# Optimization experiments

Measured on AMD Instinct MI355X. Metric: run time of the kernel, lower is better.

Reference implementation:

```python
import jax, jax.numpy as jnp
import numpy as np

HEADS = 16
DIM_HEAD = 64
DIM = 1024
INNER = HEADS * DIM_HEAD  # 1024
DIM_OUT = 1024


def setup_inputs() -> dict:
    key = jax.random.key(0)
    k1, k2, k3, k4 = jax.random.split(key, 4)
    B, N = 4, 2048
    x = jax.random.normal(k1, (B, N, DIM), dtype=jnp.float32)
    # hk.Linear(inner_dim*3, with_bias=False): weight shape [in, out]
    w_qkv = jax.random.normal(k2, (DIM, INNER * 3), dtype=jnp.float32) / np.sqrt(DIM)
    # hk.Linear(dim_out): weight [INNER, DIM_OUT] + bias
    w_out = jax.random.normal(k3, (INNER, DIM_OUT), dtype=jnp.float32) / np.sqrt(INNER)
    b_out = jax.random.normal(k4, (DIM_OUT,), dtype=jnp.float32) * 0.01
    return {"x": x, "w_qkv": w_qkv, "w_out": w_out, "b_out": b_out}


def reference(x, w_qkv, w_out, b_out):
    B, N, _ = x.shape
    scale = DIM_HEAD ** -0.5
    qkv = x @ w_qkv  # [B, N, 3*INNER]
    q, k, v = jnp.split(qkv, 3, axis=-1)
    # b n (h d) -> b h n d
    split_heads = lambda t: t.reshape(B, N, HEADS, DIM_HEAD).transpose(0, 2, 1, 3)
    q, k, v = split_heads(q), split_heads(k), split_heads(v)
    dots = jnp.einsum('bhid,bhjd->bhij', q, k) * scale  # [B, H, N, N]
    attn = jax.nn.softmax(dots, axis=-1)
    out = jnp.einsum('bhij,bhjd->bhid', attn, v)  # [B, H, N, D]
    out = out.transpose(0, 2, 1, 3).reshape(B, N, INNER)  # b h n d -> b n (h d)
    return out @ w_out + b_out
```

## Files before the change

### kernel.cpp

```cpp
#include <hip/hip_runtime.h>
#include <cstdint>


typedef unsigned short ushort_t;
typedef _Float16 half_t;
typedef half_t half8 __attribute__((ext_vector_type(8)));
typedef half_t half4 __attribute__((ext_vector_type(4)));
typedef __fp16 fp16x2 __attribute__((ext_vector_type(2)));
typedef float floatx4 __attribute__((ext_vector_type(4)));
typedef ushort_t ushort8 __attribute__((ext_vector_type(8)));

#define QSCALE 0.18033688011112043f

__device__ __forceinline__ float bf2f(ushort_t h) {
  union { unsigned int u; float f; } v; v.u = ((unsigned int)h) << 16; return v.f;
}
__device__ __forceinline__ void async_copy16(const void* g, void* l) {
  __builtin_amdgcn_global_load_lds(
      reinterpret_cast<const __attribute__((address_space(1))) unsigned int*>(
          reinterpret_cast<uintptr_t>(g)),
      reinterpret_cast<__attribute__((address_space(3))) unsigned int*>(
          reinterpret_cast<uintptr_t>(l)),
      16, 0, 0);
}
__device__ __forceinline__ void lds_fence() {
  asm volatile("s_waitcnt lgkmcnt(0)" ::: "memory");
}
__device__ __forceinline__ void vm_fence() {
  asm volatile("s_waitcnt vmcnt(0)" ::: "memory");
}

__global__ __launch_bounds__(256) void prep_kernel(
    const void* __restrict__ x_raw, half_t* __restrict__ xb,
    const void* __restrict__ w_qkv_raw, half_t* __restrict__ WTqkv,
    const void* __restrict__ w_out_raw, half_t* __restrict__ WTout,
    const void* __restrict__ b_out_raw, float* __restrict__ bb) {
  __shared__ half_t tile[64][65];
  __shared__ int cnt;
  const int tid = threadIdx.x;
  if (tid == 0) cnt = 0;
  __syncthreads();
  {
    const ushort_t* xs = (const ushort_t*)x_raw;
    int local = 0;
    for (int i = tid; i < 8192; i += 256)
      if ((xs[i] & 0x7F80u) == 0x7F80u) ++local;
    if (local) atomicAdd(&cnt, local);
  }
  __syncthreads();
  const int isf32 = (cnt >= 2) ? 1 : 0;
  const int bid = blockIdx.x;

  if (bid < 4096) {
    const int i0 = (bid * 256 + tid) * 8;
    half8 o;
    if (isf32) {
      const floatx4* s = (const floatx4*)x_raw;
      const floatx4 a = s[(i0 >> 2)];
      const floatx4 b = s[(i0 >> 2) + 1];
#pragma unroll
      for (int j = 0; j < 4; ++j) { o[j] = (half_t)a[j]; o[4 + j] = (half_t)b[j]; }
    } else {
      const ushort8 u = *(const ushort8*)((const ushort_t*)x_raw + i0);
#pragma unroll
      for (int j = 0; j < 8; ++j) o[j] = (half_t)bf2f(u[j]);
    }
    *(half8*)&xb[i0] = o;
  } else if (bid < 5120) {
    const int t = bid - 4096;
    const int bx = t & 63;
    const int by = t >> 6;
    const void* src; half_t* dst; int C, c0;
    if (bx < 48) { src = w_qkv_raw; dst = WTqkv; C = 3072; c0 = bx * 64; }
    else         { src = w_out_raw; dst = WTout; C = 1024; c0 = (bx - 48) * 64; }
    const int R = 1024;
    const int r0 = by * 64;
    const int tx = tid & 63, ty = tid >> 6;
    if (isf32) {
      const float* s = (const float*)src;
      for (int i = ty; i < 64; i += 4) tile[i][tx] = (half_t)s[(size_t)(r0 + i) * C + (c0 + tx)];
    } else {
      const ushort_t* s = (const ushort_t*)src;
      for (int i = ty; i < 64; i += 4) tile[i][tx] = (half_t)bf2f(s[(size_t)(r0 + i) * C + (c0 + tx)]);
    }
    __syncthreads();
    for (int i = ty; i < 64; i += 4) dst[(size_t)(c0 + i) * R + (r0 + tx)] = tile[tx][i];
  } else {
#pragma unroll
    for (int j = 0; j < 4; ++j) {
      const int i = j * 256 + tid;
      bb[i] = isf32 ? ((const float*)b_out_raw)[i] : bf2f(((const ushort_t*)b_out_raw)[i]);
    }
  }
}

__global__ __launch_bounds__(256) void gemm_qkv_kernel(
    const half_t* __restrict__ X, const half_t* __restrict__ WT,
    half_t* __restrict__ Qb, half_t* __restrict__ Kb, half_t* __restrict__ VTb) {
  __shared__ half_t smem[128 * 136];
  half_t* As = smem;
  half_t* Bs = smem + 128 * 64;
  const int tid = threadIdx.x;
  const int wv = tid >> 6, lane = tid & 63;
  const int l15 = lane & 15, quad = lane >> 4;
  const int l7 = l15 & 7;
  const int wm = wv & 1, wn = wv >> 1;
  const int bid = blockIdx.x;
  const int xcd = bid & 7, idx = bid >> 3;
  const int mb = xcd * 8 + (idx & 7);
  const int nb = idx >> 3;
  const int rlo = lane >> 3, ci = lane & 7;
  const int sw_klo = (ci ^ rlo) * 8;

  floatx4 acc[4][4];
  const floatx4 z = {0.f, 0.f, 0.f, 0.f};
#pragma unroll
  for (int mi = 0; mi < 4; ++mi)
#pragma unroll
    for (int ni = 0; ni < 4; ++ni) acc[mi][ni] = z;

  const half_t* Abase = X + (size_t)mb * 128 * 1024;
  const half_t* Bbase = WT + (size_t)nb * 128 * 1024;

  for (int k0 = 0; k0 < 1024; k0 += 64) {
#pragma unroll
    for (int j = 0; j < 4; ++j) {
      const int rb = (wv * 4 + j) * 8;
      async_copy16(Abase + (size_t)(rb + rlo) * 1024 + k0 + sw_klo, &As[rb * 64]);
    }
#pragma unroll
    for (int j = 0; j < 4; ++j) {
      const int rb = (wv * 4 + j) * 8;
      async_copy16(Bbase + (size_t)(rb + rlo) * 1024 + k0 + sw_klo, &Bs[rb * 64]);
    }
    __syncthreads();
#pragma unroll
    for (int ks = 0; ks < 2; ++ks) {
      half8 af[4], bfv[4];
#pragma unroll
      for (int mi = 0; mi < 4; ++mi) {
        const int rr = wm * 64 + mi * 16 + l15;
        af[mi] = *(const half8*)&As[rr * 64 + (((ks * 4 + quad) ^ l7) * 8)];
      }
#pragma unroll
      for (int ni = 0; ni < 4; ++ni) {
        const int rr = wn * 64 + ni * 16 + l15;
        bfv[ni] = *(const half8*)&Bs[rr * 64 + (((ks * 4 + quad) ^ l7) * 8)];
      }
#pragma unroll
      for (int mi = 0; mi < 4; ++mi)
#pragma unroll
        for (int ni = 0; ni < 4; ++ni)
          acc[mi][ni] = __builtin_amdgcn_mfma_f32_16x16x32_f16(af[mi], bfv[ni], acc[mi][ni], 0, 0, 0);
    }
    __syncthreads();
  }

  const int which = nb >> 3;
  if (which != 2) {
    const float sc = (which == 0) ? QSCALE : 1.0f;
#pragma unroll
    for (int mi = 0; mi < 4; ++mi)
#pragma unroll
      for (int ni = 0; ni < 4; ++ni) {
        const int col = wn * 64 + ni * 16 + l15;
#pragma unroll
        for (int r = 0; r < 4; ++r) {
          const int row = wm * 64 + mi * 16 + quad * 4 + r;
          smem[row * 132 + col] = (half_t)(acc[mi][ni][r] * sc);
        }
      }
    __syncthreads();
    half_t* dstB = (which == 0) ? Qb : Kb;
    const int hbase = (nb & 7) * 2;
    const int c2 = lane * 2;
    const int hh = hbase + (c2 >> 6);
    const int dd = c2 & 63;
#pragma unroll 4
    for (int i = 0; i < 32; ++i) {
      const int row = wv * 32 + i;
      const uint32_t val = *(const uint32_t*)&smem[row * 132 + c2];
      const int rowg = mb * 128 + row;
      const int bb = rowg >> 11, nn = rowg & 2047;
      *(uint32_t*)&dstB[(((size_t)(bb * 16 + hh)) * 2048 + nn) * 64 + dd] = val;
    }
  } else {
    const int nb2 = nb - 16;
#pragma unroll
    for (int mi = 0; mi < 4; ++mi)
#pragma unroll
      for (int ni = 0; ni < 4; ++ni) {
        const int nl = wn * 64 + ni * 16 + l15;
#pragma unroll
        for (int r = 0; r < 4; ++r) {
          const int ml = wm * 64 + mi * 16 + quad * 4 + r;
          smem[nl * 136 + ml] = (half_t)acc[mi][ni][r];
        }
      }
    __syncthreads();
    const int bb = mb >> 4;
    const int nn0 = (mb * 128) & 2047;
    const int lane2 = lane * 2;
#pragma unroll 4
    for (int it = 0; it < 32; ++it) {
      const int row = it * 4 + wv;
      const int hh = nb2 * 2 + (row >> 6);
      const int dd = row & 63;
      const int keyoff = lane2 ^ ((dd & 8) ? 4 : 0);
      const uint32_t val = *(const uint32_t*)&smem[row * 136 + lane2];
      *(uint32_t*)&VTb[((size_t)((bb * 16 + hh) * 64 + dd)) * 2048 + nn0 + keyoff] = val;
    }
  }
}

__global__ __launch_bounds__(512) void attn_kernel(
    const half_t* __restrict__ Qb, const half_t* __restrict__ Kb,
    const half_t* __restrict__ VTb, half_t* __restrict__ Ob) {
  __shared__ half_t smem[16384];
  const int tid = threadIdx.x, wv = tid >> 6, lane = tid & 63;
  const int l15 = lane & 15, quad = lane >> 4;
  const int l7 = l15 & 7;
  const int bid = blockIdx.x;
  const int xcd = bid & 7, idx = bid >> 3;
  const int bh = ((idx & 7) << 3) + xcd;
  const int qt = idx >> 3;
  const int bq = bh >> 4, hh = bh & 15;
  const half_t* Qg = Qb + (size_t)bh * 2048 * 64;
  const half_t* Kg = Kb + (size_t)bh * 2048 * 64;
  const half_t* Vg = VTb + (size_t)bh * 64 * 2048;
  const int q0 = qt * 256;
  const int rlo = lane >> 3, ci = lane & 7;
  const int sw_klo = (ci ^ rlo) * 8;

  const int q1 = quad >> 1, qb0 = quad & 1, b3 = (l15 >> 3) & 1;
  int kx[2], vx[4];
#pragma unroll
  for (int ks = 0; ks < 2; ++ks) kx[ks] = ((ks * 4 + quad) ^ l7) * 8;
#pragma unroll
  for (int ki = 0; ki < 4; ++ki)
    vx[ki] = (((ki * 2 + q1) ^ l7) * 8) + ((qb0 ^ b3) * 4);

#pragma unroll
  for (int j = 0; j < 4; ++j) {
    const int rb = (wv * 4 + j) * 8;
    async_copy16(Qg + (size_t)(q0 + rb + rlo) * 64 + sw_klo, &smem[rb * 64]);
  }
  vm_fence();
  half8 aq[2][2];
#pragma unroll
  for (int ks = 0; ks < 2; ++ks)
#pragma unroll
    for (int qi = 0; qi < 2; ++qi) {
      const int rr = wv * 32 + qi * 16 + l15;
      aq[ks][qi] = *(const half8*)&smem[rr * 64 + (((ks * 4 + quad) ^ l7) * 8)];
    }
  __syncthreads();

  floatx4 o_acc[2][4];
  const floatx4 z = {0.f, 0.f, 0.f, 0.f};
  float l_st[2] = {0.f, 0.f};
#pragma unroll
  for (int qi = 0; qi < 2; ++qi)
#pragma unroll
    for (int di = 0; di < 4; ++di) o_acc[qi][di] = z;

  {
    const int rb = wv * 8;
    async_copy16(Kg + (size_t)(rb + rlo) * 64 + sw_klo, &smem[rb * 64]);
    async_copy16(Vg + (size_t)(rb + rlo) * 2048 + sw_klo, &smem[8192 + rb * 64]);
  }

#pragma unroll 2
  for (int t = 0; t < 32; ++t) {
    const int co = (t & 1) * 4096;
    const int po = 4096 - co;
    __syncthreads();
    if (t < 31) {
      const int rb = wv * 8;
      async_copy16(Kg + (size_t)((t + 1) * 64 + rb + rlo) * 64 + sw_klo,
                   &smem[po + rb * 64]);
      async_copy16(Vg + (size_t)(rb + rlo) * 2048 + (t + 1) * 64 + sw_klo,
                   &smem[8192 + po + rb * 64]);
    }
    const half_t* Kc = &smem[co];
    const half_t* Vc = &smem[8192 + co];

    floatx4 s_acc[4][2];
#pragma unroll
    for (int ki = 0; ki < 4; ++ki)
#pragma unroll
      for (int qi = 0; qi < 2; ++qi) s_acc[ki][qi] = z;
#pragma unroll
    for (int ks = 0; ks < 2; ++ks) {
      half8 bk[4];
#pragma unroll
      for (int ki = 0; ki < 4; ++ki)
        bk[ki] = *(const half8*)&Kc[(ki * 16 + l15) * 64 + kx[ks]];
      __builtin_amdgcn_s_setprio(1);
#pragma unroll
      for (int ki = 0; ki < 4; ++ki)
#pragma unroll
        for (int qi = 0; qi < 2; ++qi)
          s_acc[ki][qi] = __builtin_amdgcn_mfma_f32_16x16x32_f16(bk[ki], aq[ks][qi], s_acc[ki][qi], 0, 0, 0);
      __builtin_amdgcn_s_setprio(0);
    }

#pragma unroll
    for (int c = 0; c < 2; ++c) {
      half8 bv[4];
#pragma unroll
      for (int di = 0; di < 4; ++di) {
        union { half4 q[2]; half8 v; } b_;
        b_.q[0] = *(const half4*)&Vc[(di * 16 + l15) * 64 + vx[2 * c]];
        b_.q[1] = *(const half4*)&Vc[(di * 16 + l15) * 64 + vx[2 * c + 1]];
        bv[di] = b_.v;
      }
      union Ap { uint32_t u[4]; half8 h; } apu[2];
#pragma unroll
      for (int kii = 0; kii < 2; ++kii)
#pragma unroll
        for (int qi = 0; qi < 2; ++qi) {
          const int ki = c * 2 + kii;
          const float p0 = __builtin_amdgcn_exp2f(s_acc[ki][qi][0]);
          const float p1 = __builtin_amdgcn_exp2f(s_acc[ki][qi][1]);
          const float p2 = __builtin_amdgcn_exp2f(s_acc[ki][qi][2]);
          const float p3 = __builtin_amdgcn_exp2f(s_acc[ki][qi][3]);
          l_st[qi] += (p0 + p1) + (p2 + p3);
          union { fp16x2 v; uint32_t u; } lo_, hi_;
          lo_.v = __builtin_amdgcn_cvt_pkrtz(p0, p1);
          hi_.v = __builtin_amdgcn_cvt_pkrtz(p2, p3);
          apu[qi].u[kii * 2] = lo_.u;
          apu[qi].u[kii * 2 + 1] = hi_.u;
        }
      __builtin_amdgcn_s_setprio(1);
#pragma unroll
      for (int qi = 0; qi < 2; ++qi)
#pragma unroll
        for (int di = 0; di < 4; ++di)
          o_acc[qi][di] = __builtin_amdgcn_mfma_f32_16x16x32_f16(apu[qi].h, bv[di], o_acc[qi][di], 0, 0, 0);
      __builtin_amdgcn_s_setprio(0);
    }
  }

  float linv[2];
#pragma unroll
  for (int qi = 0; qi < 2; ++qi) {
    float rs = l_st[qi];
    rs += __shfl_xor(rs, 16);
    rs += __shfl_xor(rs, 32);
    linv[qi] = 1.0f / rs;
  }

  __syncthreads();
  const int c2 = (tid & 31) * 2;
  const int rbase = (tid >> 5) & 15;
#pragma unroll
  for (int p = 0; p < 2; ++p) {
    if ((wv >> 2) == p) {
      const int rw = (wv & 3) * 32;
#pragma unroll
      for (int qi = 0; qi < 2; ++qi)
#pragma unroll
        for (int r = 0; r < 4; ++r) {
          const float inv = __shfl(linv[qi], quad * 4 + r);
          const int rowl = rw + qi * 16 + quad * 4 + r;
#pragma unroll
          for (int di = 0; di < 4; ++di)
            smem[rowl * 72 + di * 16 + l15] = (half_t)(o_acc[qi][di][r] * inv);
        }
    }
    __syncthreads();
#pragma unroll 4
    for (int i = 0; i < 8; ++i) {
      const int rowl = i * 16 + rbase;
      const uint32_t val = *(const uint32_t*)&smem[rowl * 72 + c2];
      const int nn = q0 + p * 128 + rowl;
      *(uint32_t*)&Ob[((size_t)(bq * 2048 + nn)) * 1024 + hh * 64 + c2] = val;
    }
    __syncthreads();
  }
}

__global__ __launch_bounds__(256) void gemm_out_kernel(
    const half_t* __restrict__ A, const half_t* __restrict__ WT,
    const float* __restrict__ bias, float* __restrict__ out) {
  __shared__ half_t As[128 * 64];
  __shared__ half_t Bs[128 * 64];
  const int tid = threadIdx.x;
  const int wv = tid >> 6, lane = tid & 63;
  const int l15 = lane & 15, quad = lane >> 4;
  const int l7 = l15 & 7;
  const int wm = wv & 1, wn = wv >> 1;
  const int bid = blockIdx.x;
  const int xcd = bid & 7, idx = bid >> 3;
  const int mb = xcd * 8 + (idx & 7);
  const int nb = idx >> 3;
  const int rlo = lane >> 3, ci = lane & 7;
  const int sw_klo = (ci ^ rlo) * 8;

  floatx4 acc[4][4];
  const floatx4 z = {0.f, 0.f, 0.f, 0.f};
#pragma unroll
  for (int mi = 0; mi < 4; ++mi)
#pragma unroll
    for (int ni = 0; ni < 4; ++ni) acc[mi][ni] = z;

  const half_t* Abase = A + (size_t)mb * 128 * 1024;
  const half_t* Bbase = WT + (size_t)nb * 128 * 1024;

  for (int k0 = 0; k0 < 1024; k0 += 64) {
#pragma unroll
    for (int j = 0; j < 4; ++j) {
      const int rb = (wv * 4 + j) * 8;
      async_copy16(Abase + (size_t)(rb + rlo) * 1024 + k0 + sw_klo, &As[rb * 64]);
    }
#pragma unroll
    for (int j = 0; j < 4; ++j) {
      const int rb = (wv * 4 + j) * 8;
      async_copy16(Bbase + (size_t)(rb + rlo) * 1024 + k0 + sw_klo, &Bs[rb * 64]);
    }
    __syncthreads();
#pragma unroll
    for (int ks = 0; ks < 2; ++ks) {
      half8 af[4], bfv[4];
#pragma unroll
      for (int mi = 0; mi < 4; ++mi) {
        const int rr = wm * 64 + mi * 16 + l15;
        af[mi] = *(const half8*)&As[rr * 64 + (((ks * 4 + quad) ^ l7) * 8)];
      }
#pragma unroll
      for (int ni = 0; ni < 4; ++ni) {
        const int rr = wn * 64 + ni * 16 + l15;
        bfv[ni] = *(const half8*)&Bs[rr * 64 + (((ks * 4 + quad) ^ l7) * 8)];
      }
#pragma unroll
      for (int mi = 0; mi < 4; ++mi)
#pragma unroll
        for (int ni = 0; ni < 4; ++ni)
          acc[mi][ni] = __builtin_amdgcn_mfma_f32_16x16x32_f16(af[mi], bfv[ni], acc[mi][ni], 0, 0, 0);
    }
    __syncthreads();
  }

#pragma unroll
  for (int mi = 0; mi < 4; ++mi) {
#pragma unroll
    for (int ni = 0; ni < 4; ++ni) {
      const int colg = nb * 128 + wn * 64 + ni * 16 + l15;
      const float bs = bias[colg];
#pragma unroll
      for (int r = 0; r < 4; ++r) {
        const int rowg = mb * 128 + wm * 64 + mi * 16 + quad * 4 + r;
        out[(size_t)rowg * 1024 + colg] = acc[mi][ni][r] + bs;
      }
    }
  }
}

extern "C" void kernel_launch(void* const* d_in, const int* in_sizes, int n_in,
                              void* d_out, int out_size, void* d_ws, size_t ws_size,
                              hipStream_t stream) {
  const void* x_raw     = d_in[0];
  const void* w_qkv_raw = d_in[1];
  const void* w_out_raw = d_in[2];
  const void* b_out_raw = d_in[3];
  float* out = (float*)d_out;

  char* ws = (char*)d_ws;
  half_t* xb    = (half_t*)(ws);
  half_t* Qb    = (half_t*)(ws + ((size_t)16 << 20));
  half_t* Kb    = (half_t*)(ws + ((size_t)32 << 20));
  half_t* VTb   = (half_t*)(ws + ((size_t)48 << 20));
  half_t* WTqkv = (half_t*)(ws + ((size_t)64 << 20));
  half_t* WTout = (half_t*)(ws + ((size_t)70 << 20));
  float*  bb    = (float*)(ws + ((size_t)72 << 20));
  half_t* Ob    = xb;

  prep_kernel<<<5121, 256, 0, stream>>>(x_raw, xb, w_qkv_raw, WTqkv,
                                        w_out_raw, WTout, b_out_raw, bb);
  gemm_qkv_kernel<<<1536, 256, 0, stream>>>(xb, WTqkv, Qb, Kb, VTb);
  attn_kernel<<<512, 512, 0, stream>>>(Qb, Kb, VTb, Ob);
  gemm_out_kernel<<<512, 256, 0, stream>>>(Ob, WTout, bb, out);
}
```

Baseline: 267.6 us.

## Rewrite QKV GEMM as 256x256 tile with double-buffered interleaved async loads

The QKV projection GEMM moves from 128x128 tiles with 256 threads to 256x256 tiles with 512 threads. It double-buffers the global-to-LDS async copies, issuing loads for the next K step between the MFMA groups of the current one, and uses setprio around the MFMAs. The epilogue now writes Q/K with 16-byte stores and stages V^T in two halves. The goal is more data reuse per tile and overlap of memory with compute. In exchange it uses 128KB of LDS and many more accumulator registers, and launches only 384 blocks, which may limit occupancy and leave some CUs unevenly loaded.

Result: no change. 265.5 us (-0.8%).

```diff
diff --git a/kernel.cpp b/kernel.cpp
--- a/kernel.cpp
+++ b/kernel.cpp
@@ -94,121 +94,201 @@
   }
 }
 
-__global__ __launch_bounds__(256) void gemm_qkv_kernel(
+__global__ __launch_bounds__(512) void gemm_qkv_kernel(
     const half_t* __restrict__ X, const half_t* __restrict__ WT,
     half_t* __restrict__ Qb, half_t* __restrict__ Kb, half_t* __restrict__ VTb) {
-  __shared__ half_t smem[128 * 136];
-  half_t* As = smem;
-  half_t* Bs = smem + 128 * 64;
+  __shared__ half_t smem[65536];
   const int tid = threadIdx.x;
   const int wv = tid >> 6, lane = tid & 63;
-  const int l15 = lane & 15, quad = lane >> 4;
-  const int l7 = l15 & 7;
+  const int l15 = lane & 15, quad = lane >> 4, l7 = l15 & 7;
   const int wm = wv & 1, wn = wv >> 1;
   const int bid = blockIdx.x;
   const int xcd = bid & 7, idx = bid >> 3;
-  const int mb = xcd * 8 + (idx & 7);
-  const int nb = idx >> 3;
+  const int mb = xcd * 4 + (idx & 3);
+  const int nb = idx >> 2;
   const int rlo = lane >> 3, ci = lane & 7;
   const int sw_klo = (ci ^ rlo) * 8;
-
-  floatx4 acc[4][4];
+  const int rb0 = wv * 16, rb1 = wv * 16 + 8;
+
+  const half_t* Ah[2] = {X + (size_t)(mb * 256) * 1024,
+                         X + (size_t)(mb * 256 + 128) * 1024};
+  const half_t* Bh[2] = {WT + (size_t)(nb * 256) * 1024,
+                         WT + (size_t)(nb * 256 + 128) * 1024};
+
+  floatx4 acc[8][4];
   const floatx4 z = {0.f, 0.f, 0.f, 0.f};
 #pragma unroll
-  for (int mi = 0; mi < 4; ++mi)
+  for (int mi = 0; mi < 8; ++mi)
 #pragma unroll
     for (int ni = 0; ni < 4; ++ni) acc[mi][ni] = z;
 
-  const half_t* Abase = X + (size_t)mb * 128 * 1024;
-  const half_t* Bbase = WT + (size_t)nb * 128 * 1024;
-
-  for (int k0 = 0; k0 < 1024; k0 += 64) {
-#pragma unroll
-    for (int j = 0; j < 4; ++j) {
-      const int rb = (wv * 4 + j) * 8;
-      async_copy16(Abase + (size_t)(rb + rlo) * 1024 + k0 + sw_klo, &As[rb * 64]);
-    }
-#pragma unroll
-    for (int j = 0; j < 4; ++j) {
-      const int rb = (wv * 4 + j) * 8;
-      async_copy16(Bbase + (size_t)(rb + rlo) * 1024 + k0 + sw_klo, &Bs[rb * 64]);
-    }
-    __syncthreads();
-#pragma unroll
-    for (int ks = 0; ks < 2; ++ks) {
-      half8 af[4], bfv[4];
-#pragma unroll
-      for (int mi = 0; mi < 4; ++mi) {
-        const int rr = wm * 64 + mi * 16 + l15;
-        af[mi] = *(const half8*)&As[rr * 64 + (((ks * 4 + quad) ^ l7) * 8)];
-      }
-#pragma unroll
-      for (int ni = 0; ni < 4; ++ni) {
-        const int rr = wn * 64 + ni * 16 + l15;
-        bfv[ni] = *(const half8*)&Bs[rr * 64 + (((ks * 4 + quad) ^ l7) * 8)];
-      }
-#pragma unroll
-      for (int mi = 0; mi < 4; ++mi)
-#pragma unroll
-        for (int ni = 0; ni < 4; ++ni)
-          acc[mi][ni] = __builtin_amdgcn_mfma_f32_16x16x32_f16(af[mi], bfv[ni], acc[mi][ni], 0, 0, 0);
-    }
-    __syncthreads();
-  }
-
-  const int which = nb >> 3;
+#pragma unroll
+  for (int h = 0; h < 2; ++h) {
+    async_copy16(Ah[h] + (size_t)(rb0 + rlo) * 1024 + sw_klo, &smem[h * 8192 + rb0 * 64]);
+    async_copy16(Ah[h] + (size_t)(rb1 + rlo) * 1024 + sw_klo, &smem[h * 8192 + rb1 * 64]);
+  }
+#pragma unroll
+  for (int h = 0; h < 2; ++h) {
+    async_copy16(Bh[h] + (size_t)(rb0 + rlo) * 1024 + sw_klo, &smem[16384 + h * 8192 + rb0 * 64]);
+    async_copy16(Bh[h] + (size_t)(rb1 + rlo) * 1024 + sw_klo, &smem[16384 + h * 8192 + rb1 * 64]);
+  }
+
+#pragma unroll 2
+  for (int u = 0; u < 16; ++u) {
+    const int b = u & 1, bn = b ^ 1;
+    const int kn = ((u + 1) & 15) * 64;
+    const int cb = b * 32768, cn = bn * 32768;
+
+    async_copy16(Ah[0] + (size_t)(rb0 + rlo) * 1024 + kn + sw_klo, &smem[cn + rb0 * 64]);
+    async_copy16(Ah[0] + (size_t)(rb1 + rlo) * 1024 + kn + sw_klo, &smem[cn + rb1 * 64]);
+    asm volatile("s_waitcnt vmcnt(2)" ::: "memory");
+    __builtin_amdgcn_s_barrier();
+    __builtin_amdgcn_sched_barrier(0);
+
+    half8 bf[4][2];
+    const int bbase = cb + 16384 + (wn >> 1) * 8192 + ((wn & 1) * 64) * 64;
+#pragma unroll
+    for (int ni = 0; ni < 4; ++ni)
+#pragma unroll
+      for (int ks = 0; ks < 2; ++ks)
+        bf[ni][ks] = *(const half8*)&smem[bbase + (ni * 16 + l15) * 64 + (((ks * 4 + quad) ^ l7) * 8)];
+    const int abase = cb + wm * 8192;
+    {
+      half8 af[2][2];
+#pragma unroll
+      for (int m2 = 0; m2 < 2; ++m2)
+#pragma unroll
+        for (int ks = 0; ks < 2; ++ks)
+          af[m2][ks] = *(const half8*)&smem[abase + ((0 * 2 + m2) * 16 + l15) * 64 + (((ks * 4 + quad) ^ l7) * 8)];
+      __builtin_amdgcn_s_setprio(1);
+#pragma unroll
+      for (int ks = 0; ks < 2; ++ks)
+#pragma unroll
+        for (int m2 = 0; m2 < 2; ++m2)
+#pragma unroll
+          for (int ni = 0; ni < 4; ++ni)
+            acc[0 * 2 + m2][ni] = __builtin_amdgcn_mfma_f32_16x16x32_f16(af[m2][ks], bf[ni][ks], acc[0 * 2 + m2][ni], 0, 0, 0);
+      __builtin_amdgcn_s_setprio(0);
+    }
+    async_copy16(Ah[1] + (size_t)(rb0 + rlo) * 1024 + kn + sw_klo, &smem[cn + 8192 + rb0 * 64]);
+    async_copy16(Ah[1] + (size_t)(rb1 + rlo) * 1024 + kn + sw_klo, &smem[cn + 8192 + rb1 * 64]);
+    {
+      half8 af[2][2];
+#pragma unroll
+      for (int m2 = 0; m2 < 2; ++m2)
+#pragma unroll
+        for (int ks = 0; ks < 2; ++ks)
+          af[m2][ks] = *(const half8*)&smem[abase + ((1 * 2 + m2) * 16 + l15) * 64 + (((ks * 4 + quad) ^ l7) * 8)];
+      __builtin_amdgcn_s_setprio(1);
+#pragma unroll
+      for (int ks = 0; ks < 2; ++ks)
+#pragma unroll
+        for (int m2 = 0; m2 < 2; ++m2)
+#pragma unroll
+          for (int ni = 0; ni < 4; ++ni)
+            acc[1 * 2 + m2][ni] = __builtin_amdgcn_mfma_f32_16x16x32_f16(af[m2][ks], bf[ni][ks], acc[1 * 2 + m2][ni], 0, 0, 0);
+      __builtin_amdgcn_s_setprio(0);
+    }
+    async_copy16(Bh[0] + (size_t)(rb0 + rlo) * 1024 + kn + sw_klo, &smem[cn + 16384 + rb0 * 64]);
+    async_copy16(Bh[0] + (size_t)(rb1 + rlo) * 1024 + kn + sw_klo, &smem[cn + 16384 + rb1 * 64]);
+    {
+      half8 af[2][2];
+#pragma unroll
+      for (int m2 = 0; m2 < 2; ++m2)
+#pragma unroll
+        for (int ks = 0; ks < 2; ++ks)
+          af[m2][ks] = *(const half8*)&smem[abase + ((2 * 2 + m2) * 16 + l15) * 64 + (((ks * 4 + quad) ^ l7) * 8)];
+      __builtin_amdgcn_s_setprio(1);
+#pragma unroll
+      for (int ks = 0; ks < 2; ++ks)
+#pragma unroll
+        for (int m2 = 0; m2 < 2; ++m2)
+#pragma unroll
+          for (int ni = 0; ni < 4; ++ni)
+            acc[2 * 2 + m2][ni] = __builtin_amdgcn_mfma_f32_16x16x32_f16(af[m2][ks], bf[ni][ks], acc[2 * 2 + m2][ni], 0, 0, 0);
+      __builtin_amdgcn_s_setprio(0);
+    }
+    async_copy16(Bh[1] + (size_t)(rb0 + rlo) * 1024 + kn + sw_klo, &smem[cn + 24576 + rb0 * 64]);
+    async_copy16(Bh[1] + (size_t)(rb1 + rlo) * 1024 + kn + sw_klo, &smem[cn + 24576 + rb1 * 64]);
+    {
+      half8 af[2][2];
+#pragma unroll
+      for (int m2 = 0; m2 < 2; ++m2)
+#pragma unroll
+        for (int ks = 0; ks < 2; ++ks)
+          af[m2][ks] = *(const half8*)&smem[abase + ((3 * 2 + m2) * 16 + l15) * 64 + (((ks * 4 + quad) ^ l7) * 8)];
+      __builtin_amdgcn_s_setprio(1);
+#pragma unroll
+      for (int ks = 0; ks < 2; ++ks)
+#pragma unroll
+        for (int m2 = 0; m2 < 2; ++m2)
+#pragma unroll
+          for (int ni = 0; ni < 4; ++ni)
+            acc[3 * 2 + m2][ni] = __builtin_amdgcn_mfma_f32_16x16x32_f16(af[m2][ks], bf[ni][ks], acc[3 * 2 + m2][ni], 0, 0, 0);
+      __builtin_amdgcn_s_setprio(0);
+    }
+  }
+
+  vm_fence();
+  __syncthreads();
+
+  const int which = nb >> 2;
   if (which != 2) {
     const float sc = (which == 0) ? QSCALE : 1.0f;
 #pragma unroll
-    for (int mi = 0; mi < 4; ++mi)
+    for (int mi = 0; mi < 8; ++mi)
 #pragma unroll
       for (int ni = 0; ni < 4; ++ni) {
         const int col = wn * 64 + ni * 16 + l15;
-#pragma unroll
-        for (int r = 0; r < 4; ++r) {
-          const int row = wm * 64 + mi * 16 + quad * 4 + r;
-          smem[row * 132 + col] = (half_t)(acc[mi][ni][r] * sc);
-        }
+        const int rowb = wm * 128 + mi * 16 + quad * 4;
+#pragma unroll
+        for (int r = 0; r < 4; ++r)
+          smem[(rowb + r) * 256 + col] = (half_t)(acc[mi][ni][r] * sc);
       }
     __syncthreads();
     half_t* dstB = (which == 0) ? Qb : Kb;
-    const int hbase = (nb & 7) * 2;
-    const int c2 = lane * 2;
-    const int hh = hbase + (c2 >> 6);
-    const int dd = c2 & 63;
+    const int seg = tid & 31;
+    const int hh = (nb & 3) * 4 + (seg >> 3);
+    const int dd = (seg & 7) * 8;
 #pragma unroll 4
-    for (int i = 0; i < 32; ++i) {
-      const int row = wv * 32 + i;
-      const uint32_t val = *(const uint32_t*)&smem[row * 132 + c2];
-      const int rowg = mb * 128 + row;
+    for (int i = 0; i < 16; ++i) {
+      const int row = i * 16 + (tid >> 5);
+      const half8 val = *(const half8*)&smem[row * 256 + seg * 8];
+      const int rowg = mb * 256 + row;
       const int bb = rowg >> 11, nn = rowg & 2047;
-      *(uint32_t*)&dstB[(((size_t)(bb * 16 + hh)) * 2048 + nn) * 64 + dd] = val;
+      *(half8*)&dstB[(((size_t)(bb * 16 + hh)) * 2048 + nn) * 64 + dd] = val;
     }
   } else {
-    const int nb2 = nb - 16;
-#pragma unroll
-    for (int mi = 0; mi < 4; ++mi)
-#pragma unroll
-      for (int ni = 0; ni < 4; ++ni) {
-        const int nl = wn * 64 + ni * 16 + l15;
-#pragma unroll
-        for (int r = 0; r < 4; ++r) {
-          const int ml = wm * 64 + mi * 16 + quad * 4 + r;
-          smem[nl * 136 + ml] = (half_t)acc[mi][ni][r];
-        }
-      }
-    __syncthreads();
-    const int bb = mb >> 4;
-    const int nn0 = (mb * 128) & 2047;
-    const int lane2 = lane * 2;
+    const int nb2 = nb - 8;
+    const int bb = mb >> 3;
+    const int nn0 = (mb * 256) & 2047;
+#pragma unroll
+    for (int q = 0; q < 2; ++q) {
+      if ((wn >> 1) == q) {
+        const int dlb = (wn & 1) * 64;
+#pragma unroll
+        for (int mi = 0; mi < 8; ++mi)
+#pragma unroll
+          for (int ni = 0; ni < 4; ++ni) {
+            const int dl = dlb + ni * 16 + l15;
+            const int rowb = wm * 128 + mi * 16 + quad * 4;
+#pragma unroll
+            for (int r = 0; r < 4; ++r)
+              smem[dl * 264 + rowb + r] = (half_t)acc[mi][ni][r];
+          }
+      }
+      __syncthreads();
+      const int npos = (tid & 127) * 2;
 #pragma unroll 4
-    for (int it = 0; it < 32; ++it) {
-      const int row = it * 4 + wv;
-      const int hh = nb2 * 2 + (row >> 6);
-      const int dd = row & 63;
-      const int keyoff = lane2 ^ ((dd & 8) ? 4 : 0);
-      const uint32_t val = *(const uint32_t*)&smem[row * 136 + lane2];
-      *(uint32_t*)&VTb[((size_t)((bb * 16 + hh) * 64 + dd)) * 2048 + nn0 + keyoff] = val;
+      for (int i = 0; i < 32; ++i) {
+        const int dl = i * 4 + (tid >> 7);
+        const int hh = nb2 * 4 + q * 2 + (dl >> 6);
+        const int dd = dl & 63;
+        const int koff = npos ^ ((dd & 8) ? 4 : 0);
+        const uint32_t val = *(const uint32_t*)&smem[dl * 264 + npos];
+        *(uint32_t*)&VTb[((size_t)((bb * 16 + hh) * 64 + dd)) * 2048 + nn0 + koff] = val;
+      }
+      __syncthreads();
     }
   }
 }
@@ -478,7 +558,7 @@
 
   prep_kernel<<<5121, 256, 0, stream>>>(x_raw, xb, w_qkv_raw, WTqkv,
                                         w_out_raw, WTout, b_out_raw, bb);
-  gemm_qkv_kernel<<<1536, 256, 0, stream>>>(xb, WTqkv, Qb, Kb, VTb);
+  gemm_qkv_kernel<<<384, 512, 0, stream>>>(xb, WTqkv, Qb, Kb, VTb);
   attn_kernel<<<512, 512, 0, stream>>>(Qb, Kb, VTb, Ob);
   gemm_out_kernel<<<512, 256, 0, stream>>>(Ob, WTout, bb, out);
 }
```
